# Performance work log

Hardware: AMD Instinct MI355X
Metric: run time of the kernel (lower is better)

Reference implementation:

```python
import jax, jax.numpy as jnp
import numpy as np

N_HEAD = 16
D_MODEL = 1024
B, C = 4, 2048

def setup_inputs() -> dict:
    key = jax.random.key(0)
    k_x, k_wq, k_bq, k_wo, k_bo = jax.random.split(key, 5)
    s = 0.02
    return {
        "x": jax.random.normal(k_x, (B, C, D_MODEL), dtype=jnp.float32),
        "W_qkv": jax.random.normal(k_wq, (D_MODEL, 3 * D_MODEL), dtype=jnp.float32) * s,
        "b_qkv": jax.random.normal(k_bq, (3 * D_MODEL,), dtype=jnp.float32) * s,
        "W_o": jax.random.normal(k_wo, (D_MODEL, D_MODEL), dtype=jnp.float32) * s,
        "b_o": jax.random.normal(k_bo, (D_MODEL,), dtype=jnp.float32) * s,
    }

def reference(x, W_qkv, b_qkv, W_o, b_o):
    Bsz, Cq, D = x.shape
    H = N_HEAD
    hd = D // H
    qkv = x @ W_qkv + b_qkv                      # [B,C,3D]
    Q, K, V = jnp.split(qkv, 3, axis=2)
    # [B,C,H,hd] -> [B,H,C,hd]
    Q = Q.reshape(Bsz, Cq, H, hd).transpose(0, 2, 1, 3)
    K = K.reshape(Bsz, Cq, H, hd).transpose(0, 2, 1, 3)
    V = V.reshape(Bsz, Cq, H, hd).transpose(0, 2, 1, 3)
    scale = 1.0 / np.sqrt(hd).astype(np.float32)
    att = jnp.einsum('bhqd,bhkd->bhqk', Q, K) * scale
    causal = jnp.tril(jnp.ones((Cq, Cq), dtype=bool))
    att = jnp.where(causal, att, jnp.float32(-jnp.inf))
    att = jax.nn.softmax(att, axis=-1)           # dropout = identity (eval)
    out = jnp.einsum('bhqk,bhkd->bhqd', att, V)  # [B,H,C,hd]
    out = out.transpose(0, 2, 1, 3).reshape(Bsz, Cq, D)
    return out @ W_o + b_o
```

## Files before the change

### kernel.cpp

```cpp
#include <hip/hip_runtime.h>
#include <hip/hip_bf16.h>

typedef __attribute__((ext_vector_type(8))) short bf16x8;
typedef __attribute__((ext_vector_type(4))) float f32x4;

#define NH 16
#define DM 1024
#define HD 64
#define CSEQ 2048
#define MROWS 8192
#define NBH 64

static __device__ __forceinline__ unsigned short f2bf(float f) {
  __hip_bfloat16 h = __float2bfloat16(f);
  return *reinterpret_cast<unsigned short*>(&h);
}

static __device__ __forceinline__ short bf_qscale(short s) {
  unsigned u = ((unsigned)(unsigned short)s) << 16;
  float f = __builtin_bit_cast(float, u) * 0.18033688f;
  return (short)f2bf(f);
}

static __device__ __forceinline__ void gload_lds16(const void* g, void* l) {
  __builtin_amdgcn_global_load_lds(
      (const __attribute__((address_space(1))) unsigned int*)g,
      (__attribute__((address_space(3))) unsigned int*)l, 16, 0, 0);
}

__global__ __launch_bounds__(256) void cast_f32_bf16(const float* __restrict__ in,
                                                     unsigned short* __restrict__ out,
                                                     int n4) {
  int stride = gridDim.x * blockDim.x;
  for (int i = blockIdx.x * blockDim.x + threadIdx.x; i < n4; i += stride) {
    float4 v = ((const float4*)in)[i];
    ushort4 o;
    o.x = f2bf(v.x); o.y = f2bf(v.y); o.z = f2bf(v.z); o.w = f2bf(v.w);
    ((ushort4*)out)[i] = o;
  }
}

__global__ __launch_bounds__(256) void transpose_cast(const float* __restrict__ src,
                                                      unsigned short* __restrict__ dst,
                                                      int K, int N) {
  __shared__ float tile[32][33];
  int tx = threadIdx.x, ty = threadIdx.y;
  int n0 = blockIdx.x * 32, k0 = blockIdx.y * 32;
  #pragma unroll
  for (int i = 0; i < 32; i += 8)
    tile[ty + i][tx] = src[(size_t)(k0 + ty + i) * N + n0 + tx];
  __syncthreads();
  #pragma unroll
  for (int i = 0; i < 32; i += 8)
    dst[(size_t)(n0 + ty + i) * K + k0 + tx] = f2bf(tile[tx][ty + i]);
}


template<int CNT>
static __device__ __forceinline__ void ld_frags(const char* base, int r0, int cx, int g,
                                                bf16x8 (*out)[2]) {
  #pragma unroll
  for (int i = 0; i < CNT; i++) {
    int row = r0 + i * 16 + cx;
    #pragma unroll
    for (int kc = 0; kc < 2; kc++)
      out[i][kc] = *(const bf16x8*)(base + row * 128 + ((((kc << 2) | g) ^ (row & 7)) << 4));
  }
}

static __device__ __forceinline__ void mfma_pair(const bf16x8 af[4][2], const bf16x8 bf2[2][2],
                                                 f32x4 acc[4][4], int n0) {
  #pragma unroll
  for (int kc = 0; kc < 2; kc++)
    #pragma unroll
    for (int mi = 0; mi < 4; mi++)
      #pragma unroll
      for (int ni = 0; ni < 2; ni++)
        acc[mi][n0 + ni] = __builtin_amdgcn_mfma_f32_16x16x32_bf16(
            af[mi][kc], bf2[ni][kc], acc[mi][n0 + ni], 0, 0, 0);
}

#define BARR() __builtin_amdgcn_s_barrier()
#define LGKM0() asm volatile("s_waitcnt lgkmcnt(0)" ::: "memory")
#define VMCNT8() asm volatile("s_waitcnt vmcnt(8)" ::: "memory")
#define VMCNT0() asm volatile("s_waitcnt vmcnt(0)" ::: "memory")
#define PRIO1() __builtin_amdgcn_s_setprio(1)
#define PRIO0() __builtin_amdgcn_s_setprio(0)

template<int MODE>
__global__ __launch_bounds__(256, 2) void gemm128d(const unsigned short* __restrict__ A,
                                                   const unsigned short* __restrict__ BT,
                                                   const float* __restrict__ bias,
                                                   float* __restrict__ outF,
                                                   unsigned short* __restrict__ outQKV,
                                                   int N, int K) {
  __shared__ char sA[2][16384];
  __shared__ char sB[2][16384];
  int tid = threadIdx.x;
  int w = tid >> 6, l = tid & 63, g = l >> 4, cx = l & 15;
  int wm = (w >> 1) * 64, wn = (w & 1) * 64;

  int nwgx = gridDim.x;
  int nwg = nwgx * gridDim.y;
  int gid = blockIdx.y * nwgx + blockIdx.x;
  int swz = (gid & 7) * (nwg >> 3) + (gid >> 3);
  int bm = (swz / nwgx) * 128, bn = (swz % nwgx) * 128;

  const unsigned short* Ap[4];
  const unsigned short* Bp[4];
  #pragma unroll
  for (int i = 0; i < 4; i++) {
    int c = tid + i * 256;
    int ar = c >> 3, as = ((c & 7) ^ (ar & 7)) * 8;
    Ap[i] = A + (size_t)(bm + ar) * K + as;
    Bp[i] = BT + (size_t)(bn + ar) * K + as;
  }

  #define STAGE_AB(t, buf) do { int ko_ = (t) << 6;                 \
      gload_lds16(Ap[0] + ko_, sA[buf] + (tid)       * 16);         \
      gload_lds16(Ap[1] + ko_, sA[buf] + (tid + 256) * 16);         \
      gload_lds16(Ap[2] + ko_, sA[buf] + (tid + 512) * 16);         \
      gload_lds16(Ap[3] + ko_, sA[buf] + (tid + 768) * 16);         \
      gload_lds16(Bp[0] + ko_, sB[buf] + (tid)       * 16);         \
      gload_lds16(Bp[1] + ko_, sB[buf] + (tid + 256) * 16);         \
      gload_lds16(Bp[2] + ko_, sB[buf] + (tid + 512) * 16);         \
      gload_lds16(Bp[3] + ko_, sB[buf] + (tid + 768) * 16);         \
    } while (0)

  f32x4 acc[4][4];
  #pragma unroll
  for (int i = 0; i < 4; i++)
    #pragma unroll
    for (int j = 0; j < 4; j++) acc[i][j] = (f32x4){0.f, 0.f, 0.f, 0.f};

  int NT = K >> 6;

  STAGE_AB(0, 0);
  STAGE_AB(1, 1);
  VMCNT8();
  BARR();

  int cur = 0;
  for (int t = 0; t < NT; t++) {
    const char* Ac = sA[cur];
    const char* Bc = sB[cur];
    bool h1 = (t + 1) < NT, h2 = (t + 2) < NT;
    bf16x8 af[4][2], bfr[4][2];

    ld_frags<4>(Ac, wm, cx, g, af);
    ld_frags<4>(Bc, wn, cx, g, bfr);
    BARR(); LGKM0();
    PRIO1(); mfma_pair(af, &bfr[0], acc, 0); PRIO0();
    BARR();

    if (h2) STAGE_AB(t + 2, cur);
    PRIO1(); mfma_pair(af, &bfr[2], acc, 2); PRIO0();
    if (h2)      { VMCNT8(); }
    else if (h1) { VMCNT0(); }
    BARR();
    cur ^= 1;
  }

  #pragma unroll
  for (int mi = 0; mi < 4; mi++) {
    #pragma unroll
    for (int ni = 0; ni < 4; ni++) {
      int col = bn + wn + ni * 16 + cx;
      float bv = bias[col];
      int row0 = bm + wm + mi * 16 + g * 4;
      #pragma unroll
      for (int r = 0; r < 4; r++) {
        float v = acc[mi][ni][r] + bv;
        int rr = row0 + r;
        if (MODE == 0) {
          outF[(size_t)rr * N + col] = v;
        } else {
          int which = col >> 10, rem = col & 1023;
          int h = rem >> 6, d = rem & 63;
          int b = rr >> 11, cq = rr & 2047;
          if (which == 2) {
            int pos = (cq & ~31) + (((cq >> 2) & 3) << 3) + (((cq >> 4) & 1) << 2) + (cq & 3);
            outQKV[((size_t)2 * NBH + b * NH + h) * (CSEQ * HD) +
                   (size_t)d * CSEQ + pos] = f2bf(v);
          } else {
            outQKV[((size_t)which * NBH + b * NH + h) * (CSEQ * HD) + (size_t)cq * HD + d] = f2bf(v);
          }
        }
      }
    }
  }
  #undef STAGE_AB
}

__global__ __launch_bounds__(512, 4) void attn_kernel(const unsigned short* __restrict__ Qb,
                                                      const unsigned short* __restrict__ Kb,
                                                      const unsigned short* __restrict__ VTb,
                                                      unsigned short* __restrict__ O) {
  __shared__ char sKb[2][16384];
  __shared__ char sVt[2][16384];
  int tid = threadIdx.x;
  int w = tid >> 6, l = tid & 63, g = l >> 4, cx = l & 15;
  int gid = blockIdx.x;
  int bh = ((gid >> 7) << 3) | (gid & 7);
  int qt = 15 - ((gid >> 3) & 15);

  const unsigned short* Qp  = Qb  + (size_t)bh * CSEQ * HD;
  const unsigned short* Kp  = Kb  + (size_t)bh * CSEQ * HD;
  const unsigned short* VTp = VTb + (size_t)bh * CSEQ * HD;

  int qrow = qt * 128 + w * 16 + cx;
  bf16x8 qf[2];
  qf[0] = *(const bf16x8*)(Qp + (size_t)qrow * HD + g * 8);
  qf[1] = *(const bf16x8*)(Qp + (size_t)qrow * HD + 32 + g * 8);
  #pragma unroll
  for (int kc = 0; kc < 2; kc++)
    #pragma unroll
    for (int j = 0; j < 8; j++) qf[kc][j] = bf_qscale(qf[kc][j]);

  f32x4 o[4];
  #pragma unroll
  for (int nf2 = 0; nf2 < 4; nf2++) o[nf2] = (f32x4){0.f, 0.f, 0.f, 0.f};
  float mrow = -INFINITY, lrow = 0.f;

  int c0 = tid, c1 = tid + 512;
  int krow0 = c0 >> 3, ksl0 = (c0 & 7) ^ (krow0 & 7);
  int krow1 = c1 >> 3, ksl1 = (c1 & 7) ^ (krow1 & 7);
  int vd0 = c0 >> 4, vsl0 = (c0 & 15) ^ (vd0 & 7);
  int vd1 = c1 >> 4, vsl1 = (c1 & 15) ^ (vd1 & 7);
  const unsigned short* Ksrc0 = Kp + (size_t)krow0 * HD + ksl0 * 8;
  const unsigned short* Ksrc1 = Kp + (size_t)krow1 * HD + ksl1 * 8;
  const unsigned short* Vsrc0 = VTp + (size_t)vd0 * CSEQ + vsl0 * 8;
  const unsigned short* Vsrc1 = VTp + (size_t)vd1 * CSEQ + vsl1 * 8;

  gload_lds16(Ksrc0, sKb[0] + c0 * 16);
  gload_lds16(Ksrc1, sKb[0] + c1 * 16);
  gload_lds16(Vsrc0, sVt[0] + c0 * 16);
  gload_lds16(Vsrc1, sVt[0] + c1 * 16);
  __syncthreads();
  int cur = 0;

  for (int kt = 0; kt <= qt; kt++) {
    if (kt < qt) {
      size_t ko = (size_t)(kt + 1) * 128 * HD;
      size_t vo = (size_t)(kt + 1) * 128;
      gload_lds16(Ksrc0 + ko, sKb[cur ^ 1] + c0 * 16);
      gload_lds16(Ksrc1 + ko, sKb[cur ^ 1] + c1 * 16);
      gload_lds16(Vsrc0 + vo, sVt[cur ^ 1] + c0 * 16);
      gload_lds16(Vsrc1 + vo, sVt[cur ^ 1] + c1 * 16);
    }
    const char* Kc = sKb[cur];
    const char* Vc = sVt[cur];

    f32x4 sacc[8];
    #pragma unroll
    for (int nf = 0; nf < 8; nf++) sacc[nf] = (f32x4){0.f, 0.f, 0.f, 0.f};
    __builtin_amdgcn_s_setprio(1);
    #pragma unroll
    for (int kc = 0; kc < 2; kc++) {
      #pragma unroll
      for (int nf = 0; nf < 8; nf++) {
        int row = nf * 16 + cx;
        bf16x8 kf = *(const bf16x8*)(Kc + row * 128 + ((((kc << 2) | g) ^ (row & 7)) << 4));
        sacc[nf] = __builtin_amdgcn_mfma_f32_16x16x32_bf16(kf, qf[kc], sacc[nf], 0, 0, 0);
      }
    }
    __builtin_amdgcn_s_setprio(0);

    if (kt == qt) {
      #pragma unroll
      for (int nf = 0; nf < 8; nf++)
        #pragma unroll
        for (int r = 0; r < 4; r++)
          if (nf * 16 + 4 * g + r > w * 16 + cx) sacc[nf][r] = -INFINITY;
    }
    float m8[8];
    #pragma unroll
    for (int nf = 0; nf < 8; nf++)
      m8[nf] = fmaxf(fmaxf(sacc[nf][0], sacc[nf][1]), fmaxf(sacc[nf][2], sacc[nf][3]));
    float mx = fmaxf(fmaxf(fmaxf(m8[0], m8[1]), fmaxf(m8[2], m8[3])),
                     fmaxf(fmaxf(m8[4], m8[5]), fmaxf(m8[6], m8[7])));
    mx = fmaxf(mx, __shfl_xor(mx, 16));
    mx = fmaxf(mx, __shfl_xor(mx, 32));

    if (!__all(mx - mrow <= 8.f)) {
      float mnew = fmaxf(mrow, mx);
      float alpha = __builtin_amdgcn_exp2f(mrow - mnew);
      mrow = mnew;
      lrow *= alpha;
      #pragma unroll
      for (int r = 0; r < 4; r++) {
        float ar = __shfl(alpha, (l & 48) | ((l >> 2) & 12) | r);
        #pragma unroll
        for (int nf2 = 0; nf2 < 4; nf2++) o[nf2][r] *= ar;
      }
    }
    #pragma unroll
    for (int nf = 0; nf < 8; nf++)
      #pragma unroll
      for (int r = 0; r < 4; r++)
        sacc[nf][r] = __builtin_amdgcn_exp2f(sacc[nf][r] - mrow);
    float s8[8];
    #pragma unroll
    for (int nf = 0; nf < 8; nf++)
      s8[nf] = (sacc[nf][0] + sacc[nf][1]) + (sacc[nf][2] + sacc[nf][3]);
    float sum = ((s8[0] + s8[1]) + (s8[2] + s8[3])) + ((s8[4] + s8[5]) + (s8[6] + s8[7]));
    sum += __shfl_xor(sum, 16);
    sum += __shfl_xor(sum, 32);
    lrow += sum;

    bf16x8 pa[4];
    #pragma unroll
    for (int kc = 0; kc < 4; kc++) {
      #pragma unroll
      for (int j = 0; j < 4; j++) {
        pa[kc][j]     = (short)f2bf(sacc[2 * kc][j]);
        pa[kc][j + 4] = (short)f2bf(sacc[2 * kc + 1][j]);
      }
    }

    __builtin_amdgcn_s_setprio(1);
    #pragma unroll
    for (int kc = 0; kc < 4; kc++) {
      #pragma unroll
      for (int nf2 = 0; nf2 < 4; nf2++) {
        int d = nf2 * 16 + cx;
        bf16x8 vf = *(const bf16x8*)(Vc + ((d * 256 + (((kc << 2) | g) << 4)) ^ ((d & 7) << 4)));
        o[nf2] = __builtin_amdgcn_mfma_f32_16x16x32_bf16(pa[kc], vf, o[nf2], 0, 0, 0);
      }
    }
    __builtin_amdgcn_s_setprio(0);

    if (kt < qt) {
      __syncthreads();
      cur ^= 1;
    }
  }

  int b = bh >> 4, h = bh & 15;
  float linv = 1.0f / lrow;
  #pragma unroll
  for (int r = 0; r < 4; r++) {
    float inv = __shfl(linv, (l & 48) | ((l >> 2) & 12) | r);
    int q = qt * 128 + w * 16 + 4 * g + r;
    size_t base = ((size_t)(b * CSEQ + q)) * DM + h * HD;
    #pragma unroll
    for (int nf2 = 0; nf2 < 4; nf2++)
      O[base + nf2 * 16 + cx] = f2bf(o[nf2][r] * inv);
  }
}

extern "C" void kernel_launch(void* const* d_in, const int* in_sizes, int n_in,
                              void* d_out, int out_size, void* d_ws, size_t ws_size,
                              hipStream_t stream) {
  const float* x    = (const float*)d_in[0];
  const float* Wqkv = (const float*)d_in[1];
  const float* bqkv = (const float*)d_in[2];
  const float* Wo   = (const float*)d_in[3];
  const float* bo   = (const float*)d_in[4];
  float* out = (float*)d_out;

  unsigned short* ws = (unsigned short*)d_ws;
  const size_t XB_OFF    = 0;
  const size_t WQKVT_OFF = 8388608;
  const size_t WOT_OFF   = WQKVT_OFF + 3145728;
  const size_t QKV_OFF   = WOT_OFF + 1048576;
  const size_t ATT_OFF   = QKV_OFF + 3 * 8388608;

  unsigned short* xb    = ws + XB_OFF;
  unsigned short* wqkvT = ws + WQKVT_OFF;
  unsigned short* woT   = ws + WOT_OFF;
  unsigned short* qkv   = ws + QKV_OFF;
  unsigned short* att   = ws + ATT_OFF;

  cast_f32_bf16<<<2048, 256, 0, stream>>>(x, xb, (MROWS * DM) / 4);
  transpose_cast<<<dim3(3 * DM / 32, DM / 32), dim3(32, 8), 0, stream>>>(Wqkv, wqkvT, DM, 3 * DM);
  transpose_cast<<<dim3(DM / 32, DM / 32), dim3(32, 8), 0, stream>>>(Wo, woT, DM, DM);

  gemm128d<1><<<dim3(3 * DM / 128, MROWS / 128), 256, 0, stream>>>(
      xb, wqkvT, bqkv, nullptr, qkv, 3 * DM, DM);

  attn_kernel<<<dim3(1024), 512, 0, stream>>>(
      qkv, qkv + 8388608, qkv + 16777216, att);

  gemm128d<0><<<dim3(DM / 128, MROWS / 128), 256, 0, stream>>>(
      att, woT, bo, out, nullptr, DM, DM);
}
```

Before: 197.0 us.

## Use 256x256-tile, 8-wave pipelined GEMM for the QKV projection

Adds a new gemm256p kernel with 256x256 output tiles, 512 threads, and double-buffered 64-deep K stages. Each half-iteration splits the MFMA work into quadrants, with global-to-LDS prefetch interleaved between them. It replaces the 128x128 kernel only for the QKV projection, aiming for more operand reuse per LDS load and less global traffic. The catch is fewer workgroups (12x32=384) and 128 KB of LDS per block, so occupancy drops and wave quantization on the CUs may get worse.

```diff
diff --git a/kernel.cpp b/kernel.cpp
--- a/kernel.cpp
+++ b/kernel.cpp
@@ -55,7 +55,6 @@
     dst[(size_t)(n0 + ty + i) * K + k0 + tx] = f2bf(tile[tx][ty + i]);
 }
 
-
 template<int CNT>
 static __device__ __forceinline__ void ld_frags(const char* base, int r0, int cx, int g,
                                                 bf16x8 (*out)[2]) {
@@ -66,18 +65,6 @@
     for (int kc = 0; kc < 2; kc++)
       out[i][kc] = *(const bf16x8*)(base + row * 128 + ((((kc << 2) | g) ^ (row & 7)) << 4));
   }
-}
-
-static __device__ __forceinline__ void mfma_pair(const bf16x8 af[4][2], const bf16x8 bf2[2][2],
-                                                 f32x4 acc[4][4], int n0) {
-  #pragma unroll
-  for (int kc = 0; kc < 2; kc++)
-    #pragma unroll
-    for (int mi = 0; mi < 4; mi++)
-      #pragma unroll
-      for (int ni = 0; ni < 2; ni++)
-        acc[mi][n0 + ni] = __builtin_amdgcn_mfma_f32_16x16x32_bf16(
-            af[mi][kc], bf2[ni][kc], acc[mi][n0 + ni], 0, 0, 0);
 }
 
 #define BARR() __builtin_amdgcn_s_barrier()
@@ -86,6 +73,151 @@
 #define VMCNT0() asm volatile("s_waitcnt vmcnt(0)" ::: "memory")
 #define PRIO1() __builtin_amdgcn_s_setprio(1)
 #define PRIO0() __builtin_amdgcn_s_setprio(0)
+
+
+static __device__ __forceinline__ void mfma_q16(const bf16x8 af[4][2], const bf16x8 bq[2][2],
+                                                f32x4 (*acc)[4], int m0, int n0) {
+  #pragma unroll
+  for (int kc = 0; kc < 2; kc++)
+    #pragma unroll
+    for (int mi = 0; mi < 4; mi++)
+      #pragma unroll
+      for (int ni = 0; ni < 2; ni++)
+        acc[m0 + mi][n0 + ni] = __builtin_amdgcn_mfma_f32_16x16x32_bf16(
+            af[mi][kc], bq[ni][kc], acc[m0 + mi][n0 + ni], 0, 0, 0);
+}
+
+template<int MODE>
+__global__ __launch_bounds__(512, 2) void gemm256p(const unsigned short* __restrict__ A,
+                                                   const unsigned short* __restrict__ BT,
+                                                   const float* __restrict__ bias,
+                                                   float* __restrict__ outF,
+                                                   unsigned short* __restrict__ outQKV,
+                                                   int N, int K) {
+  __shared__ char sA[2][32768];
+  __shared__ char sB[2][32768];
+  int tid = threadIdx.x;
+  int w = tid >> 6, l = tid & 63, g = l >> 4, cx = l & 15;
+  int wm = (w >> 2) * 128, wn = (w & 3) * 64;
+
+  int nwgx = gridDim.x;
+  int nwg = nwgx * gridDim.y;
+  int gid = blockIdx.y * nwgx + blockIdx.x;
+  int swz = (gid & 7) * (nwg >> 3) + (gid >> 3);
+  int bm = (swz / nwgx) * 256, bn = (swz % nwgx) * 256;
+
+  int c0 = tid, c1 = tid + 512;
+  int ar0 = c0 >> 3, as0 = ((c0 & 7) ^ (ar0 & 7)) * 8;
+  int ar1 = c1 >> 3, as1 = ((c1 & 7) ^ (ar1 & 7)) * 8;
+  const unsigned short* Ap0 = A + (size_t)(bm + ar0) * K + as0;
+  const unsigned short* Ap1 = A + (size_t)(bm + ar1) * K + as1;
+  const unsigned short* Bp0 = BT + (size_t)(bn + ar0) * K + as0;
+  const unsigned short* Bp1 = BT + (size_t)(bn + ar1) * K + as1;
+  const size_t HS = (size_t)128 * K;
+
+  #define SG_A(t, slot) do { int ko_ = (t) << 6;                         \
+      gload_lds16(Ap0 + ko_,      sA[slot] + c0 * 16);                   \
+      gload_lds16(Ap1 + ko_,      sA[slot] + c1 * 16);                   \
+      gload_lds16(Ap0 + HS + ko_, sA[slot] + 16384 + c0 * 16);           \
+      gload_lds16(Ap1 + HS + ko_, sA[slot] + 16384 + c1 * 16); } while (0)
+  #define SG_B(t, slot) do { int ko_ = (t) << 6;                         \
+      gload_lds16(Bp0 + ko_,      sB[slot] + c0 * 16);                   \
+      gload_lds16(Bp1 + ko_,      sB[slot] + c1 * 16);                   \
+      gload_lds16(Bp0 + HS + ko_, sB[slot] + 16384 + c0 * 16);           \
+      gload_lds16(Bp1 + HS + ko_, sB[slot] + 16384 + c1 * 16); } while (0)
+
+  f32x4 acc[8][4];
+  #pragma unroll
+  for (int i = 0; i < 8; i++)
+    #pragma unroll
+    for (int j = 0; j < 4; j++) acc[i][j] = (f32x4){0.f, 0.f, 0.f, 0.f};
+
+  int NT = K >> 6;
+  int NIT = NT >> 1;
+
+  SG_A(0, 0); SG_B(0, 0);
+  SG_A(1, 1); SG_B(1, 1);
+  VMCNT8();
+  BARR();
+
+  for (int i = 0; i < NIT; i++) {
+    int T = 2 * i;
+    bf16x8 af[4][2], bl[2][2], bh[2][2];
+    #pragma unroll
+    for (int half = 0; half < 2; half++) {
+      const char* Ac = sA[half];
+      const char* Bc = sB[half];
+      int ts = T + 2 + half;
+      bool st = ts < NT;
+
+      ld_frags<4>(Ac, wm, cx, g, af);
+      ld_frags<2>(Bc, wn, cx, g, bl);
+      BARR(); LGKM0();
+      PRIO1(); mfma_q16(af, bl, acc, 0, 0); PRIO0();
+      BARR();
+
+      ld_frags<2>(Bc, wn + 32, cx, g, bh);
+      BARR(); LGKM0();
+      PRIO1(); mfma_q16(af, bh, acc, 0, 2); PRIO0();
+      BARR();
+
+      ld_frags<4>(Ac, wm + 64, cx, g, af);
+      if (st) SG_B(ts, half);
+      BARR(); LGKM0();
+      PRIO1(); mfma_q16(af, bl, acc, 4, 0); PRIO0();
+      BARR();
+
+      if (st) SG_A(ts, half);
+      BARR();
+      PRIO1(); mfma_q16(af, bh, acc, 4, 2); PRIO0();
+      if (st) { VMCNT8(); } else { VMCNT0(); }
+      BARR();
+    }
+  }
+
+  #pragma unroll
+  for (int ai = 0; ai < 8; ai++) {
+    #pragma unroll
+    for (int aj = 0; aj < 4; aj++) {
+      int col = bn + wn + aj * 16 + cx;
+      float bv = bias[col];
+      int row0 = bm + wm + ai * 16 + g * 4;
+      #pragma unroll
+      for (int r = 0; r < 4; r++) {
+        float v = acc[ai][aj][r] + bv;
+        int rr = row0 + r;
+        if (MODE == 0) {
+          outF[(size_t)rr * N + col] = v;
+        } else {
+          int which = col >> 10, rem = col & 1023;
+          int h = rem >> 6, d = rem & 63;
+          int b = rr >> 11, cq = rr & 2047;
+          if (which == 2) {
+            int pos = (cq & ~31) + (((cq >> 2) & 3) << 3) + (((cq >> 4) & 1) << 2) + (cq & 3);
+            outQKV[((size_t)2 * NBH + b * NH + h) * (CSEQ * HD) +
+                   (size_t)d * CSEQ + pos] = f2bf(v);
+          } else {
+            outQKV[((size_t)which * NBH + b * NH + h) * (CSEQ * HD) + (size_t)cq * HD + d] = f2bf(v);
+          }
+        }
+      }
+    }
+  }
+  #undef SG_A
+  #undef SG_B
+}
+
+static __device__ __forceinline__ void mfma_pair(const bf16x8 af[4][2], const bf16x8 bf2[2][2],
+                                                 f32x4 acc[4][4], int n0) {
+  #pragma unroll
+  for (int kc = 0; kc < 2; kc++)
+    #pragma unroll
+    for (int mi = 0; mi < 4; mi++)
+      #pragma unroll
+      for (int ni = 0; ni < 2; ni++)
+        acc[mi][n0 + ni] = __builtin_amdgcn_mfma_f32_16x16x32_bf16(
+            af[mi][kc], bf2[ni][kc], acc[mi][n0 + ni], 0, 0, 0);
+}
 
 template<int MODE>
 __global__ __launch_bounds__(256, 2) void gemm128d(const unsigned short* __restrict__ A,
@@ -376,7 +508,7 @@
   transpose_cast<<<dim3(3 * DM / 32, DM / 32), dim3(32, 8), 0, stream>>>(Wqkv, wqkvT, DM, 3 * DM);
   transpose_cast<<<dim3(DM / 32, DM / 32), dim3(32, 8), 0, stream>>>(Wo, woT, DM, DM);
 
-  gemm128d<1><<<dim3(3 * DM / 128, MROWS / 128), 256, 0, stream>>>(
+  gemm256p<1><<<dim3(3 * DM / 256, MROWS / 256), 512, 0, stream>>>(
       xb, wqkvT, bqkv, nullptr, qkv, 3 * DM, DM);
 
   attn_kernel<<<dim3(1024), 512, 0, stream>>>(
```

After: 206.3 us. +4.7%, slower.

## Give each attention wave two 16-row query tiles, reusing K/V fragments

Applied to the files above, without the earlier changes.

The attention kernel now runs with 256 threads (4 waves) per block instead of 512, and each wave processes 32 query rows as two 16-row halves. Every K and V fragment read from LDS feeds two MFMAs, which halves LDS traffic per MFMA and halves the number of block barriers per unit of work. The cost is more registers per wave (doubled score and output accumulators) and the launch bound drops from 4 to 2 blocks per CU. That lowers occupancy and may cause register pressure or spills.

```diff
diff --git a/kernel.cpp b/kernel.cpp
--- a/kernel.cpp
+++ b/kernel.cpp
@@ -55,7 +55,6 @@
     dst[(size_t)(n0 + ty + i) * K + k0 + tx] = f2bf(tile[tx][ty + i]);
 }
 
-
 template<int CNT>
 static __device__ __forceinline__ void ld_frags(const char* base, int r0, int cx, int g,
                                                 bf16x8 (*out)[2]) {
@@ -66,18 +65,6 @@
     for (int kc = 0; kc < 2; kc++)
       out[i][kc] = *(const bf16x8*)(base + row * 128 + ((((kc << 2) | g) ^ (row & 7)) << 4));
   }
-}
-
-static __device__ __forceinline__ void mfma_pair(const bf16x8 af[4][2], const bf16x8 bf2[2][2],
-                                                 f32x4 acc[4][4], int n0) {
-  #pragma unroll
-  for (int kc = 0; kc < 2; kc++)
-    #pragma unroll
-    for (int mi = 0; mi < 4; mi++)
-      #pragma unroll
-      for (int ni = 0; ni < 2; ni++)
-        acc[mi][n0 + ni] = __builtin_amdgcn_mfma_f32_16x16x32_bf16(
-            af[mi][kc], bf2[ni][kc], acc[mi][n0 + ni], 0, 0, 0);
 }
 
 #define BARR() __builtin_amdgcn_s_barrier()
@@ -86,6 +73,18 @@
 #define VMCNT0() asm volatile("s_waitcnt vmcnt(0)" ::: "memory")
 #define PRIO1() __builtin_amdgcn_s_setprio(1)
 #define PRIO0() __builtin_amdgcn_s_setprio(0)
+
+static __device__ __forceinline__ void mfma_pair(const bf16x8 af[4][2], const bf16x8 bf2[2][2],
+                                                 f32x4 acc[4][4], int n0) {
+  #pragma unroll
+  for (int kc = 0; kc < 2; kc++)
+    #pragma unroll
+    for (int mi = 0; mi < 4; mi++)
+      #pragma unroll
+      for (int ni = 0; ni < 2; ni++)
+        acc[mi][n0 + ni] = __builtin_amdgcn_mfma_f32_16x16x32_bf16(
+            af[mi][kc], bf2[ni][kc], acc[mi][n0 + ni], 0, 0, 0);
+}
 
 template<int MODE>
 __global__ __launch_bounds__(256, 2) void gemm128d(const unsigned short* __restrict__ A,
@@ -192,7 +191,7 @@
   #undef STAGE_AB
 }
 
-__global__ __launch_bounds__(512, 4) void attn_kernel(const unsigned short* __restrict__ Qb,
+__global__ __launch_bounds__(256, 2) void attn_kernel(const unsigned short* __restrict__ Qb,
                                                       const unsigned short* __restrict__ Kb,
                                                       const unsigned short* __restrict__ VTb,
                                                       unsigned short* __restrict__ O) {
@@ -208,34 +207,44 @@
   const unsigned short* Kp  = Kb  + (size_t)bh * CSEQ * HD;
   const unsigned short* VTp = VTb + (size_t)bh * CSEQ * HD;
 
-  int qrow = qt * 128 + w * 16 + cx;
-  bf16x8 qf[2];
-  qf[0] = *(const bf16x8*)(Qp + (size_t)qrow * HD + g * 8);
-  qf[1] = *(const bf16x8*)(Qp + (size_t)qrow * HD + 32 + g * 8);
-  #pragma unroll
-  for (int kc = 0; kc < 2; kc++)
-    #pragma unroll
-    for (int j = 0; j < 8; j++) qf[kc][j] = bf_qscale(qf[kc][j]);
-
-  f32x4 o[4];
-  #pragma unroll
-  for (int nf2 = 0; nf2 < 4; nf2++) o[nf2] = (f32x4){0.f, 0.f, 0.f, 0.f};
-  float mrow = -INFINITY, lrow = 0.f;
-
-  int c0 = tid, c1 = tid + 512;
-  int krow0 = c0 >> 3, ksl0 = (c0 & 7) ^ (krow0 & 7);
-  int krow1 = c1 >> 3, ksl1 = (c1 & 7) ^ (krow1 & 7);
-  int vd0 = c0 >> 4, vsl0 = (c0 & 15) ^ (vd0 & 7);
-  int vd1 = c1 >> 4, vsl1 = (c1 & 15) ^ (vd1 & 7);
-  const unsigned short* Ksrc0 = Kp + (size_t)krow0 * HD + ksl0 * 8;
-  const unsigned short* Ksrc1 = Kp + (size_t)krow1 * HD + ksl1 * 8;
-  const unsigned short* Vsrc0 = VTp + (size_t)vd0 * CSEQ + vsl0 * 8;
-  const unsigned short* Vsrc1 = VTp + (size_t)vd1 * CSEQ + vsl1 * 8;
-
-  gload_lds16(Ksrc0, sKb[0] + c0 * 16);
-  gload_lds16(Ksrc1, sKb[0] + c1 * 16);
-  gload_lds16(Vsrc0, sVt[0] + c0 * 16);
-  gload_lds16(Vsrc1, sVt[0] + c1 * 16);
+  bf16x8 qf[2][2];
+  #pragma unroll
+  for (int qh = 0; qh < 2; qh++) {
+    int qrow = qt * 128 + w * 32 + qh * 16 + cx;
+    qf[qh][0] = *(const bf16x8*)(Qp + (size_t)qrow * HD + g * 8);
+    qf[qh][1] = *(const bf16x8*)(Qp + (size_t)qrow * HD + 32 + g * 8);
+    #pragma unroll
+    for (int kc = 0; kc < 2; kc++)
+      #pragma unroll
+      for (int j = 0; j < 8; j++) qf[qh][kc][j] = bf_qscale(qf[qh][kc][j]);
+  }
+
+  f32x4 o[2][4];
+  #pragma unroll
+  for (int qh = 0; qh < 2; qh++)
+    #pragma unroll
+    for (int nf2 = 0; nf2 < 4; nf2++) o[qh][nf2] = (f32x4){0.f, 0.f, 0.f, 0.f};
+  float mrow[2] = {-INFINITY, -INFINITY}, lrow[2] = {0.f, 0.f};
+
+  const unsigned short* Ksrc[4];
+  const unsigned short* Vsrc[4];
+  #pragma unroll
+  for (int i = 0; i < 4; i++) {
+    int c = tid + i * 256;
+    int krow = c >> 3, ksl = (c & 7) ^ (krow & 7);
+    int vd = c >> 4, vsl = (c & 15) ^ (vd & 7);
+    Ksrc[i] = Kp + (size_t)krow * HD + ksl * 8;
+    Vsrc[i] = VTp + (size_t)vd * CSEQ + vsl * 8;
+  }
+
+  #define ATT_STAGE(koff, voff, buf) do {                              \
+      _Pragma("unroll")                                                \
+      for (int i_ = 0; i_ < 4; i_++) {                                 \
+        gload_lds16(Ksrc[i_] + (koff), sKb[buf] + (tid + i_ * 256) * 16); \
+        gload_lds16(Vsrc[i_] + (voff), sVt[buf] + (tid + i_ * 256) * 16); \
+      } } while (0)
+
+  ATT_STAGE((size_t)0, (size_t)0, 0);
   __syncthreads();
   int cur = 0;
 
@@ -243,92 +252,109 @@
     if (kt < qt) {
       size_t ko = (size_t)(kt + 1) * 128 * HD;
       size_t vo = (size_t)(kt + 1) * 128;
-      gload_lds16(Ksrc0 + ko, sKb[cur ^ 1] + c0 * 16);
-      gload_lds16(Ksrc1 + ko, sKb[cur ^ 1] + c1 * 16);
-      gload_lds16(Vsrc0 + vo, sVt[cur ^ 1] + c0 * 16);
-      gload_lds16(Vsrc1 + vo, sVt[cur ^ 1] + c1 * 16);
+      ATT_STAGE(ko, vo, cur ^ 1);
     }
     const char* Kc = sKb[cur];
     const char* Vc = sVt[cur];
 
-    f32x4 sacc[8];
-    #pragma unroll
-    for (int nf = 0; nf < 8; nf++) sacc[nf] = (f32x4){0.f, 0.f, 0.f, 0.f};
-    __builtin_amdgcn_s_setprio(1);
+    f32x4 sacc[2][8];
+    #pragma unroll
+    for (int qh = 0; qh < 2; qh++)
+      #pragma unroll
+      for (int nf = 0; nf < 8; nf++) sacc[qh][nf] = (f32x4){0.f, 0.f, 0.f, 0.f};
+    PRIO1();
     #pragma unroll
     for (int kc = 0; kc < 2; kc++) {
       #pragma unroll
       for (int nf = 0; nf < 8; nf++) {
         int row = nf * 16 + cx;
         bf16x8 kf = *(const bf16x8*)(Kc + row * 128 + ((((kc << 2) | g) ^ (row & 7)) << 4));
-        sacc[nf] = __builtin_amdgcn_mfma_f32_16x16x32_bf16(kf, qf[kc], sacc[nf], 0, 0, 0);
+        sacc[0][nf] = __builtin_amdgcn_mfma_f32_16x16x32_bf16(kf, qf[0][kc], sacc[0][nf], 0, 0, 0);
+        sacc[1][nf] = __builtin_amdgcn_mfma_f32_16x16x32_bf16(kf, qf[1][kc], sacc[1][nf], 0, 0, 0);
       }
     }
-    __builtin_amdgcn_s_setprio(0);
+    PRIO0();
 
     if (kt == qt) {
+      #pragma unroll
+      for (int qh = 0; qh < 2; qh++)
+        #pragma unroll
+        for (int nf = 0; nf < 8; nf++)
+          #pragma unroll
+          for (int r = 0; r < 4; r++)
+            if (nf * 16 + 4 * g + r > w * 32 + qh * 16 + cx) sacc[qh][nf][r] = -INFINITY;
+    }
+    float mx[2];
+    #pragma unroll
+    for (int qh = 0; qh < 2; qh++) {
+      float m8[8];
+      #pragma unroll
+      for (int nf = 0; nf < 8; nf++)
+        m8[nf] = fmaxf(fmaxf(sacc[qh][nf][0], sacc[qh][nf][1]), fmaxf(sacc[qh][nf][2], sacc[qh][nf][3]));
+      float m = fmaxf(fmaxf(fmaxf(m8[0], m8[1]), fmaxf(m8[2], m8[3])),
+                      fmaxf(fmaxf(m8[4], m8[5]), fmaxf(m8[6], m8[7])));
+      m = fmaxf(m, __shfl_xor(m, 16));
+      m = fmaxf(m, __shfl_xor(m, 32));
+      mx[qh] = m;
+    }
+
+    float need = fmaxf(mx[0] - mrow[0], mx[1] - mrow[1]);
+    if (!__all(need <= 8.f)) {
+      #pragma unroll
+      for (int qh = 0; qh < 2; qh++) {
+        float mnew = fmaxf(mrow[qh], mx[qh]);
+        float alpha = __builtin_amdgcn_exp2f(mrow[qh] - mnew);
+        mrow[qh] = mnew;
+        lrow[qh] *= alpha;
+        #pragma unroll
+        for (int r = 0; r < 4; r++) {
+          float ar = __shfl(alpha, (l & 48) | ((l >> 2) & 12) | r);
+          #pragma unroll
+          for (int nf2 = 0; nf2 < 4; nf2++) o[qh][nf2][r] *= ar;
+        }
+      }
+    }
+    #pragma unroll
+    for (int qh = 0; qh < 2; qh++) {
       #pragma unroll
       for (int nf = 0; nf < 8; nf++)
         #pragma unroll
         for (int r = 0; r < 4; r++)
-          if (nf * 16 + 4 * g + r > w * 16 + cx) sacc[nf][r] = -INFINITY;
-    }
-    float m8[8];
-    #pragma unroll
-    for (int nf = 0; nf < 8; nf++)
-      m8[nf] = fmaxf(fmaxf(sacc[nf][0], sacc[nf][1]), fmaxf(sacc[nf][2], sacc[nf][3]));
-    float mx = fmaxf(fmaxf(fmaxf(m8[0], m8[1]), fmaxf(m8[2], m8[3])),
-                     fmaxf(fmaxf(m8[4], m8[5]), fmaxf(m8[6], m8[7])));
-    mx = fmaxf(mx, __shfl_xor(mx, 16));
-    mx = fmaxf(mx, __shfl_xor(mx, 32));
-
-    if (!__all(mx - mrow <= 8.f)) {
-      float mnew = fmaxf(mrow, mx);
-      float alpha = __builtin_amdgcn_exp2f(mrow - mnew);
-      mrow = mnew;
-      lrow *= alpha;
-      #pragma unroll
-      for (int r = 0; r < 4; r++) {
-        float ar = __shfl(alpha, (l & 48) | ((l >> 2) & 12) | r);
+          sacc[qh][nf][r] = __builtin_amdgcn_exp2f(sacc[qh][nf][r] - mrow[qh]);
+      float s8[8];
+      #pragma unroll
+      for (int nf = 0; nf < 8; nf++)
+        s8[nf] = (sacc[qh][nf][0] + sacc[qh][nf][1]) + (sacc[qh][nf][2] + sacc[qh][nf][3]);
+      float sum = ((s8[0] + s8[1]) + (s8[2] + s8[3])) + ((s8[4] + s8[5]) + (s8[6] + s8[7]));
+      sum += __shfl_xor(sum, 16);
+      sum += __shfl_xor(sum, 32);
+      lrow[qh] += sum;
+    }
+
+    bf16x8 pa[2][4];
+    #pragma unroll
+    for (int qh = 0; qh < 2; qh++)
+      #pragma unroll
+      for (int kc = 0; kc < 4; kc++) {
         #pragma unroll
-        for (int nf2 = 0; nf2 < 4; nf2++) o[nf2][r] *= ar;
+        for (int j = 0; j < 4; j++) {
+          pa[qh][kc][j]     = (short)f2bf(sacc[qh][2 * kc][j]);
+          pa[qh][kc][j + 4] = (short)f2bf(sacc[qh][2 * kc + 1][j]);
+        }
       }
-    }
-    #pragma unroll
-    for (int nf = 0; nf < 8; nf++)
-      #pragma unroll
-      for (int r = 0; r < 4; r++)
-        sacc[nf][r] = __builtin_amdgcn_exp2f(sacc[nf][r] - mrow);
-    float s8[8];
-    #pragma unroll
-    for (int nf = 0; nf < 8; nf++)
-      s8[nf] = (sacc[nf][0] + sacc[nf][1]) + (sacc[nf][2] + sacc[nf][3]);
-    float sum = ((s8[0] + s8[1]) + (s8[2] + s8[3])) + ((s8[4] + s8[5]) + (s8[6] + s8[7]));
-    sum += __shfl_xor(sum, 16);
-    sum += __shfl_xor(sum, 32);
-    lrow += sum;
-
-    bf16x8 pa[4];
-    #pragma unroll
-    for (int kc = 0; kc < 4; kc++) {
-      #pragma unroll
-      for (int j = 0; j < 4; j++) {
-        pa[kc][j]     = (short)f2bf(sacc[2 * kc][j]);
-        pa[kc][j + 4] = (short)f2bf(sacc[2 * kc + 1][j]);
-      }
-    }
-
-    __builtin_amdgcn_s_setprio(1);
+
+    PRIO1();
     #pragma unroll
     for (int kc = 0; kc < 4; kc++) {
       #pragma unroll
       for (int nf2 = 0; nf2 < 4; nf2++) {
         int d = nf2 * 16 + cx;
         bf16x8 vf = *(const bf16x8*)(Vc + ((d * 256 + (((kc << 2) | g) << 4)) ^ ((d & 7) << 4)));
-        o[nf2] = __builtin_amdgcn_mfma_f32_16x16x32_bf16(pa[kc], vf, o[nf2], 0, 0, 0);
+        o[0][nf2] = __builtin_amdgcn_mfma_f32_16x16x32_bf16(pa[0][kc], vf, o[0][nf2], 0, 0, 0);
+        o[1][nf2] = __builtin_amdgcn_mfma_f32_16x16x32_bf16(pa[1][kc], vf, o[1][nf2], 0, 0, 0);
       }
     }
-    __builtin_amdgcn_s_setprio(0);
+    PRIO0();
 
     if (kt < qt) {
       __syncthreads();
@@ -336,17 +362,21 @@
     }
   }
 
-  int b = bh >> 4, h = bh & 15;
-  float linv = 1.0f / lrow;
-  #pragma unroll
-  for (int r = 0; r < 4; r++) {
-    float inv = __shfl(linv, (l & 48) | ((l >> 2) & 12) | r);
-    int q = qt * 128 + w * 16 + 4 * g + r;
-    size_t base = ((size_t)(b * CSEQ + q)) * DM + h * HD;
-    #pragma unroll
-    for (int nf2 = 0; nf2 < 4; nf2++)
-      O[base + nf2 * 16 + cx] = f2bf(o[nf2][r] * inv);
-  }
+  int b = bh >> 4, hh = bh & 15;
+  #pragma unroll
+  for (int qh = 0; qh < 2; qh++) {
+    float linv = 1.0f / lrow[qh];
+    #pragma unroll
+    for (int r = 0; r < 4; r++) {
+      float inv = __shfl(linv, (l & 48) | ((l >> 2) & 12) | r);
+      int q = qt * 128 + w * 32 + qh * 16 + 4 * g + r;
+      size_t base = ((size_t)(b * CSEQ + q)) * DM + hh * HD;
+      #pragma unroll
+      for (int nf2 = 0; nf2 < 4; nf2++)
+        O[base + nf2 * 16 + cx] = f2bf(o[qh][nf2][r] * inv);
+    }
+  }
+  #undef ATT_STAGE
 }
 
 extern "C" void kernel_launch(void* const* d_in, const int* in_sizes, int n_in,
@@ -379,7 +409,7 @@
   gemm128d<1><<<dim3(3 * DM / 128, MROWS / 128), 256, 0, stream>>>(
       xb, wqkvT, bqkv, nullptr, qkv, 3 * DM, DM);
 
-  attn_kernel<<<dim3(1024), 512, 0, stream>>>(
+  attn_kernel<<<dim3(1024), 256, 0, stream>>>(
       qkv, qkv + 8388608, qkv + 16777216, att);
 
   gemm128d<0><<<dim3(DM / 128, MROWS / 128), 256, 0, stream>>>(
```

After: 205.9 us. 4.5% more time.
